# Optimization experiments

Measured on AMD Instinct MI355X. Metric: run time of the kernel, lower is better.

## Reference

```python
import jax, jax.numpy as jnp
import numpy as np

B, S, H = 2, 2048, 2048
E = 4
I = 8192
EI = I // E  # expert intermediate size
VOCAB = 100000

def setup_inputs() -> dict:
    key = jax.random.key(0)
    k1, k2, k3, k4, k5 = jax.random.split(key, 5)
    hidden_states = jax.random.normal(k1, (B, S, H), dtype=jnp.float32)
    token_ids = jax.random.randint(k2, (B, S), 0, VOCAB, dtype=jnp.int64)
    gate_proj = jax.random.normal(k3, (E, H, EI), dtype=jnp.float32) * 0.02
    up_proj = jax.random.normal(k4, (E, H, EI), dtype=jnp.float32) * 0.02
    down_proj = jax.random.normal(k5, (E, EI, H), dtype=jnp.float32) * 0.02
    return {"hidden_states": hidden_states, "token_ids": token_ids,
            "gate_proj": gate_proj, "up_proj": up_proj, "down_proj": down_proj}

def reference(hidden_states, token_ids, gate_proj, up_proj, down_proj):
    b, s, h = hidden_states.shape
    e_dim = gate_proj.shape[0]
    # token_to_expert = arange(vocab) % E  (no frequency table)
    tid = jnp.clip(token_ids, 0, VOCAB - 1)
    expert_ids = (tid % e_dim).reshape(-1)          # [T]
    x = hidden_states.reshape(-1, h)                # [T, H]
    T = x.shape[0]
    t_idx = jnp.arange(T)
    # grouped GEMM == per-token GEMM with token's expert weight; compute per-expert then select
    gate_all = jnp.einsum('td,edf->tef', x, gate_proj)   # [T, E, EI]
    up_all = jnp.einsum('td,edf->tef', x, up_proj)       # [T, E, EI]
    gate = gate_all[t_idx, expert_ids]                   # [T, EI]
    up = up_all[t_idx, expert_ids]                       # [T, EI]
    inter = jax.nn.silu(gate) * up                       # fused SwiGLU
    out_all = jnp.einsum('tf,efd->ted', inter, down_proj)  # [T, E, H]
    out = out_all[t_idx, expert_ids]                     # [T, H]
    return out.reshape(b, s, h)
```

## Files before the change

### kernel.cpp

```cpp
#include <hip/hip_runtime.h>

#define H_DIM 2048
#define EI_DIM 2048
#define NEXP 4
#define BM 144
#define SEG 1152
#define NROWS 4608
#define NTM 32
#define NKB 64
#define NB 16
#define AFRAG 576
#define WFRAG 512

typedef __attribute__((ext_vector_type(4))) float f32x4;
typedef __attribute__((ext_vector_type(8))) short bf16x8;
typedef __attribute__((ext_vector_type(4))) short bf16x4;

__device__ __forceinline__ short f2bf(float f) {
  unsigned u = __builtin_bit_cast(unsigned, f);
  u += 0x7fffu + ((u >> 16) & 1u);
  return (short)(u >> 16);
}

__device__ __forceinline__ void gload16(const void* g, void* l) {
  __builtin_amdgcn_global_load_lds(
      (const __attribute__((address_space(1))) unsigned*)g,
      (__attribute__((address_space(3))) unsigned*)l, 16, 0, 0);
}

__global__ void route_kernel(const void* __restrict__ token_ids,
                             int* __restrict__ meta, int* __restrict__ row2tok) {
  __shared__ unsigned long long wtot[4];
  const int tid = threadIdx.x;
  const int lane = tid & 63;
  const int wv = tid >> 6;

  for (int i = tid; i < NROWS; i += 256) row2tok[i] = -1;

  const int* ti32 = (const int*)token_ids;
  bool is64 = true;
  for (int i = 0; i < 16; ++i)
    if (ti32[2 * i + 1] != 0) is64 = false;

  const int base = tid * 16;
  unsigned long long pack = 0ULL;
  unsigned eps = 0;
  for (int i = 0; i < 16; ++i) {
    long long v = is64 ? ((const long long*)token_ids)[base + i]
                       : (long long)ti32[base + i];
    if (v < 0) v = 0;
    if (v > 99999) v = 99999;
    int e = (int)(v & 3);
    eps |= (unsigned)e << (2 * i);
    pack += 1ULL << (16 * e);
  }

  unsigned long long incl = pack;
  for (int off = 1; off < 64; off <<= 1) {
    unsigned long long up = __shfl_up(incl, off, 64);
    if (lane >= off) incl += up;
  }
  if (lane == 63) wtot[wv] = incl;
  __syncthreads();

  unsigned long long waveBase = 0;
  for (int w = 0; w < 4; ++w)
    if (w < wv) waveBase += wtot[w];
  const unsigned long long exclu = waveBase + incl - pack;

  if (tid == 0) {
    meta[0] = 36;
    for (int t = 0; t < 36; ++t) meta[1 + t] = t / 9;
  }

  int cur[4];
  for (int e = 0; e < 4; ++e)
    cur[e] = e * SEG + (int)((exclu >> (16 * e)) & 0xffff);
  for (int i = 0; i < 16; ++i) {
    int e = (int)((eps >> (2 * i)) & 3);
    int idx = cur[e]++;
    if (idx < (e + 1) * SEG) row2tok[idx] = base + i;
  }
}


__global__ __launch_bounds__(256) void convert_kernel(
    const float* __restrict__ gW, const float* __restrict__ uW,
    const float* __restrict__ dW, short* __restrict__ Pg,
    short* __restrict__ Pu, short* __restrict__ Pd) {
  const int mat = blockIdx.y;
  const float* src = mat == 0 ? gW : (mat == 1 ? uW : dW);
  short* dst = mat == 0 ? Pg : (mat == 1 ? Pu : Pd);
  const int tId = blockIdx.x;
  const int e = tId >> 9;
  const int nb = (tId >> 5) & 15;
  const int kb = tId & 31;
  const int tid = threadIdx.x;
  const int ks = tid >> 5;
  const int c4 = (tid & 31) * 4;
  const float* sb = src + (size_t)e * H_DIM * EI_DIM +
                    (size_t)(kb * 64 + ks * 8) * 2048 + nb * 128 + c4;
  f32x4 rv[8];
#pragma unroll
  for (int j = 0; j < 8; ++j) rv[j] = *(const f32x4*)(sb + (size_t)j * 2048);
  short* db = dst + (size_t)tId * 8192 + (ks * 128 + c4) * 8;
#pragma unroll
  for (int i = 0; i < 4; ++i) {
    bf16x8 v;
#pragma unroll
    for (int j = 0; j < 8; ++j) v[j] = f2bf(rv[j][i]);
    *(bf16x8*)(db + i * 8) = v;
  }
}

__global__ __launch_bounds__(256) void gather_pack_kernel(
    const float* __restrict__ hidden, const int* __restrict__ row2tok,
    short* __restrict__ xp) {
  const int tile = blockIdx.x;
  const int kb = blockIdx.y;
  const int tid = threadIdx.x;
  short* db = xp + ((size_t)tile * NKB + kb) * (AFRAG * 8);
#pragma unroll
  for (int q = 0; q < 3; ++q) {
    if (q == 2 && tid >= 64) break;
    const int idx = q * 256 + tid;
    const int ks = idx / 144, r = idx - ks * 144;
    const int tok = row2tok[tile * BM + r];
    bf16x8 v = {0, 0, 0, 0, 0, 0, 0, 0};
    if (tok >= 0) {
      const f32x4* s =
          (const f32x4*)(hidden + (size_t)tok * H_DIM + kb * 32 + ks * 8);
      f32x4 a = s[0], b = s[1];
      v[0] = f2bf(a[0]); v[1] = f2bf(a[1]); v[2] = f2bf(a[2]); v[3] = f2bf(a[3]);
      v[4] = f2bf(b[0]); v[5] = f2bf(b[1]); v[6] = f2bf(b[2]); v[7] = f2bf(b[3]);
    }
    *(bf16x8*)(db + idx * 8) = v;
  }
}

__global__ __launch_bounds__(256, 2) void gemm1_kernel(
    const short* __restrict__ xp, const short* __restrict__ Pg,
    const short* __restrict__ Pu, short* __restrict__ inter) {
  const int b0 = blockIdx.x;
  const int swz = (b0 & 7) * 64 + (b0 >> 3);
  const int tile = swz >> 4, nb = swz & 15;
  const int e = tile >> 3;

  __shared__ short L[2][12800];

  const int tid = threadIdx.x, lane = tid & 63, wv = tid >> 6;
  const int l15 = lane & 15, lks = lane >> 4;

  f32x4 accG[9][2] = {};
  f32x4 accU[9][2] = {};

  const short* aB = xp + (size_t)(tile * NKB) * (AFRAG * 8);
  const short* gB = Pg + (size_t)((e * NB + nb) * NKB) * (WFRAG * 8);
  const short* uB = Pu + (size_t)((e * NB + nb) * NKB) * (WFRAG * 8);

  const int wuni = (tid & 192) * 16;

#define STAGE1(kb, buf)                                                       \
  {                                                                           \
    const short* a = aB + (size_t)(kb) * (AFRAG * 8);                         \
    const short* g = gB + (size_t)(kb) * (WFRAG * 8);                         \
    const short* u = uB + (size_t)(kb) * (WFRAG * 8);                         \
    char* la = (char*)&L[buf][0];                                             \
    char* lg = (char*)&L[buf][4608];                                          \
    char* lu = (char*)&L[buf][8704];                                          \
    gload16(a + tid * 8, la + wuni);                                          \
    gload16(a + (256 + tid) * 8, la + 4096 + wuni);                           \
    if (tid < 64) gload16(a + (512 + tid) * 8, la + 8192 + wuni);             \
    gload16(g + tid * 8, lg + wuni);                                          \
    gload16(g + (256 + tid) * 8, lg + 4096 + wuni);                           \
    gload16(u + tid * 8, lu + wuni);                                          \
    gload16(u + (256 + tid) * 8, lu + 4096 + wuni);                           \
  }

  STAGE1(0, 0);
  asm volatile("s_waitcnt vmcnt(0)" ::: "memory");
  __syncthreads();

  int buf = 0;
  for (int kb = 0; kb < NKB; ++kb) {
    if (kb < NKB - 1) STAGE1(kb + 1, buf ^ 1);
    const short* As = &L[buf][0];
    const short* Gs = &L[buf][4608];
    const short* Us = &L[buf][8704];
    bf16x8 af[9], bg[2], bu[2];
#pragma unroll
    for (int m = 0; m < 9; ++m)
      af[m] = *(const bf16x8*)(As + (lks * 144 + m * 16 + l15) * 8);
#pragma unroll
    for (int n = 0; n < 2; ++n) {
      const int c = wv * 32 + n * 16 + l15;
      bg[n] = *(const bf16x8*)(Gs + (lks * 128 + c) * 8);
      bu[n] = *(const bf16x8*)(Us + (lks * 128 + c) * 8);
    }
    __builtin_amdgcn_s_setprio(1);
#pragma unroll
    for (int m = 0; m < 9; ++m)
#pragma unroll
      for (int n = 0; n < 2; ++n) {
        accG[m][n] = __builtin_amdgcn_mfma_f32_16x16x32_bf16(
            af[m], bg[n], accG[m][n], 0, 0, 0);
        accU[m][n] = __builtin_amdgcn_mfma_f32_16x16x32_bf16(
            af[m], bu[n], accU[m][n], 0, 0, 0);
      }
    __builtin_amdgcn_s_setprio(0);
    if (kb < NKB - 1) {
      asm volatile("s_waitcnt vmcnt(0)" ::: "memory");
      __syncthreads();
    }
    buf ^= 1;
  }
#undef STAGE1

#pragma unroll
  for (int n = 0; n < 2; ++n) {
    const int C = nb * 128 + wv * 32 + n * 16 + l15;
    const int kb2 = C >> 5, ks2 = (C >> 3) & 3, kj = C & 7;
    short* ib = inter + (((size_t)tile * NKB + kb2) * AFRAG + ks2 * 144) * 8 + kj;
#pragma unroll
    for (int m = 0; m < 9; ++m)
#pragma unroll
      for (int j = 0; j < 4; ++j) {
        const int r = m * 16 + (lks << 2) + j;
        const float g = accG[m][n][j], u = accU[m][n][j];
        const float s = g / (1.0f + __expf(-g));
        ib[(size_t)r * 8] = f2bf(s * u);
      }
  }
}

__global__ __launch_bounds__(256, 2) void gemm2_kernel(
    const short* __restrict__ inter, const short* __restrict__ Pd,
    const int* __restrict__ row2tok, float* __restrict__ out) {
  const int b0 = blockIdx.x;
  const int swz = (b0 & 7) * 64 + (b0 >> 3);
  const int tile = swz >> 4, nb = swz & 15;
  const int e = tile >> 3;

  __shared__ short L[2][8704];

  const int tid = threadIdx.x, lane = tid & 63, wv = tid >> 6;
  const int l15 = lane & 15, lks = lane >> 4;

  f32x4 acc[9][2] = {};

  const short* aB = inter + (size_t)(tile * NKB) * (AFRAG * 8);
  const short* dB = Pd + (size_t)((e * NB + nb) * NKB) * (WFRAG * 8);

  const int wuni = (tid & 192) * 16;

#define STAGE2(kb, buf)                                                       \
  {                                                                           \
    const short* a = aB + (size_t)(kb) * (AFRAG * 8);                         \
    const short* d = dB + (size_t)(kb) * (WFRAG * 8);                         \
    char* la = (char*)&L[buf][0];                                             \
    char* ld = (char*)&L[buf][4608];                                          \
    gload16(a + tid * 8, la + wuni);                                          \
    gload16(a + (256 + tid) * 8, la + 4096 + wuni);                           \
    if (tid < 64) gload16(a + (512 + tid) * 8, la + 8192 + wuni);             \
    gload16(d + tid * 8, ld + wuni);                                          \
    gload16(d + (256 + tid) * 8, ld + 4096 + wuni);                           \
  }

  STAGE2(0, 0);
  asm volatile("s_waitcnt vmcnt(0)" ::: "memory");
  __syncthreads();

  int buf = 0;
  for (int kb = 0; kb < NKB; ++kb) {
    if (kb < NKB - 1) STAGE2(kb + 1, buf ^ 1);
    const short* As = &L[buf][0];
    const short* Bs = &L[buf][4608];
    bf16x8 af[9], bd[2];
#pragma unroll
    for (int m = 0; m < 9; ++m)
      af[m] = *(const bf16x8*)(As + (lks * 144 + m * 16 + l15) * 8);
#pragma unroll
    for (int n = 0; n < 2; ++n)
      bd[n] = *(const bf16x8*)(Bs + (lks * 128 + wv * 32 + n * 16 + l15) * 8);
    __builtin_amdgcn_s_setprio(1);
#pragma unroll
    for (int m = 0; m < 9; ++m)
#pragma unroll
      for (int n = 0; n < 2; ++n)
        acc[m][n] = __builtin_amdgcn_mfma_f32_16x16x32_bf16(af[m], bd[n],
                                                            acc[m][n], 0, 0, 0);
    __builtin_amdgcn_s_setprio(0);
    if (kb < NKB - 1) {
      asm volatile("s_waitcnt vmcnt(0)" ::: "memory");
      __syncthreads();
    }
    buf ^= 1;
  }
#undef STAGE2

#pragma unroll
  for (int m = 0; m < 9; ++m)
#pragma unroll
    for (int j = 0; j < 4; ++j) {
      const int r = tile * BM + m * 16 + (lks << 2) + j;
      const int tok = row2tok[r];
      if (tok >= 0) {
        float* orow = out + (size_t)tok * H_DIM + nb * 128 + wv * 32 + l15;
#pragma unroll
        for (int n = 0; n < 2; ++n) orow[n * 16] = acc[m][n][j];
      }
    }
}


__global__ void gather_fb_kernel(const float* __restrict__ hidden,
                                 const int* __restrict__ row2tok,
                                 short* __restrict__ xperm) {
  const int r = blockIdx.x;
  const int tok = row2tok[r];
  const int tid = threadIdx.x;
  f32x4 a = {0.f, 0.f, 0.f, 0.f}, b = {0.f, 0.f, 0.f, 0.f};
  if (tok >= 0) {
    const f32x4* src = (const f32x4*)(hidden + (size_t)tok * H_DIM + 8 * tid);
    a = src[0];
    b = src[1];
  }
  bf16x8 v;
  v[0] = f2bf(a[0]); v[1] = f2bf(a[1]); v[2] = f2bf(a[2]); v[3] = f2bf(a[3]);
  v[4] = f2bf(b[0]); v[5] = f2bf(b[1]); v[6] = f2bf(b[2]); v[7] = f2bf(b[3]);
  *(bf16x8*)(xperm + (size_t)r * H_DIM + 8 * tid) = v;
}

__global__ __launch_bounds__(256, 2) void gemm1_fb_kernel(
    const short* __restrict__ xperm, const float* __restrict__ gateW,
    const float* __restrict__ upW, const int* __restrict__ meta,
    short* __restrict__ inter) {
  const int tm = blockIdx.x;
  if (tm >= meta[0]) return;
  const int e = meta[1 + tm];
  const int rowBase = tm * 128;
  const int colBase = blockIdx.y * 128;
  const float* gW = gateW + (size_t)e * H_DIM * EI_DIM;
  const float* uW = upW + (size_t)e * H_DIM * EI_DIM;

  __shared__ short As[128 * 64];
  __shared__ short Bg[128 * 64];
  __shared__ short Bu[128 * 64];

  const int tid = threadIdx.x;
  const int lane = tid & 63;
  const int wv = tid >> 6;
  const int wr = (wv >> 1) * 64;
  const int wc = (wv & 1) * 64;

  f32x4 accG[4][4] = {};
  f32x4 accU[4][4] = {};

  const int ar = tid >> 3;
  const int ak = (tid & 7) * 8;
  const int bn = (tid & 31) * 4;
  const int bk = (tid >> 5) * 4;

  for (int k0 = 0; k0 < H_DIM; k0 += 64) {
    bf16x8 av[4];
#pragma unroll
    for (int p = 0; p < 4; ++p) {
      int r = ar + p * 32;
      av[p] = *(const bf16x8*)(xperm + (size_t)(rowBase + r) * H_DIM + k0 + ak);
    }
    f32x4 gv[2][4], uv[2][4];
#pragma unroll
    for (int p = 0; p < 2; ++p) {
      int kk = k0 + bk + p * 32;
#pragma unroll
      for (int i = 0; i < 4; ++i) {
        gv[p][i] = *(const f32x4*)(gW + (size_t)(kk + i) * EI_DIM + colBase + bn);
        uv[p][i] = *(const f32x4*)(uW + (size_t)(kk + i) * EI_DIM + colBase + bn);
      }
    }
    __syncthreads();
#pragma unroll
    for (int p = 0; p < 4; ++p) {
      int r = ar + p * 32;
      int idx = (r * 64 + ak) ^ ((r & 7) << 3);
      *(bf16x8*)(As + idx) = av[p];
    }
#pragma unroll
    for (int p = 0; p < 2; ++p) {
      int kk = bk + p * 32;
#pragma unroll
      for (int j = 0; j < 4; ++j) {
        int rowp = bn + j;
        int idx = (rowp * 64 + kk) ^ ((rowp & 7) << 3);
        bf16x4 vg, vu;
        vg[0] = f2bf(gv[p][0][j]); vg[1] = f2bf(gv[p][1][j]);
        vg[2] = f2bf(gv[p][2][j]); vg[3] = f2bf(gv[p][3][j]);
        vu[0] = f2bf(uv[p][0][j]); vu[1] = f2bf(uv[p][1][j]);
        vu[2] = f2bf(uv[p][2][j]); vu[3] = f2bf(uv[p][3][j]);
        *(bf16x4*)(Bg + idx) = vg;
        *(bf16x4*)(Bu + idx) = vu;
      }
    }
    __syncthreads();
#pragma unroll
    for (int kk = 0; kk < 64; kk += 32) {
      const int kb = kk + ((lane >> 4) << 3);
      bf16x8 af[4], bgf[4], buf_[4];
#pragma unroll
      for (int m = 0; m < 4; ++m) {
        int r = wr + m * 16 + (lane & 15);
        af[m] = *(const bf16x8*)(As + ((r * 64 + kb) ^ ((r & 7) << 3)));
      }
#pragma unroll
      for (int n = 0; n < 4; ++n) {
        int c = wc + n * 16 + (lane & 15);
        int idx = (c * 64 + kb) ^ ((c & 7) << 3);
        bgf[n] = *(const bf16x8*)(Bg + idx);
        buf_[n] = *(const bf16x8*)(Bu + idx);
      }
#pragma unroll
      for (int m = 0; m < 4; ++m)
#pragma unroll
        for (int n = 0; n < 4; ++n) {
          accG[m][n] = __builtin_amdgcn_mfma_f32_16x16x32_bf16(
              af[m], bgf[n], accG[m][n], 0, 0, 0);
          accU[m][n] = __builtin_amdgcn_mfma_f32_16x16x32_bf16(
              af[m], buf_[n], accU[m][n], 0, 0, 0);
        }
    }
  }
#pragma unroll
  for (int m = 0; m < 4; ++m)
#pragma unroll
    for (int n = 0; n < 4; ++n) {
      int c = colBase + wc + n * 16 + (lane & 15);
#pragma unroll
      for (int j = 0; j < 4; ++j) {
        int r = rowBase + wr + m * 16 + ((lane >> 4) << 2) + j;
        float g = accG[m][n][j], u = accU[m][n][j];
        float s = g / (1.0f + __expf(-g));
        inter[(size_t)r * EI_DIM + c] = f2bf(s * u);
      }
    }
}

__global__ __launch_bounds__(256, 2) void gemm2_fb_kernel(
    const short* __restrict__ inter, const float* __restrict__ downW,
    const int* __restrict__ meta, const int* __restrict__ row2tok,
    float* __restrict__ out) {
  const int tm = blockIdx.x;
  if (tm >= meta[0]) return;
  const int e = meta[1 + tm];
  const int rowBase = tm * 128;
  const int colBase = blockIdx.y * 128;
  const float* dW = downW + (size_t)e * EI_DIM * H_DIM;

  __shared__ short As[128 * 64];
  __shared__ short Bs[128 * 64];

  const int tid = threadIdx.x;
  const int lane = tid & 63;
  const int wv = tid >> 6;
  const int wr = (wv >> 1) * 64;
  const int wc = (wv & 1) * 64;

  f32x4 acc[4][4] = {};

  const int ar = tid >> 3;
  const int ak = (tid & 7) * 8;
  const int bn = (tid & 31) * 4;
  const int bk = (tid >> 5) * 4;

  for (int k0 = 0; k0 < EI_DIM; k0 += 64) {
    bf16x8 av[4];
#pragma unroll
    for (int p = 0; p < 4; ++p) {
      int r = ar + p * 32;
      av[p] = *(const bf16x8*)(inter + (size_t)(rowBase + r) * EI_DIM + k0 + ak);
    }
    f32x4 dv[2][4];
#pragma unroll
    for (int p = 0; p < 2; ++p) {
      int kk = k0 + bk + p * 32;
#pragma unroll
      for (int i = 0; i < 4; ++i)
        dv[p][i] = *(const f32x4*)(dW + (size_t)(kk + i) * H_DIM + colBase + bn);
    }
    __syncthreads();
#pragma unroll
    for (int p = 0; p < 4; ++p) {
      int r = ar + p * 32;
      int idx = (r * 64 + ak) ^ ((r & 7) << 3);
      *(bf16x8*)(As + idx) = av[p];
    }
#pragma unroll
    for (int p = 0; p < 2; ++p) {
      int kk = bk + p * 32;
#pragma unroll
      for (int j = 0; j < 4; ++j) {
        int rowp = bn + j;
        int idx = (rowp * 64 + kk) ^ ((rowp & 7) << 3);
        bf16x4 vd;
        vd[0] = f2bf(dv[p][0][j]); vd[1] = f2bf(dv[p][1][j]);
        vd[2] = f2bf(dv[p][2][j]); vd[3] = f2bf(dv[p][3][j]);
        *(bf16x4*)(Bs + idx) = vd;
      }
    }
    __syncthreads();
#pragma unroll
    for (int kk = 0; kk < 64; kk += 32) {
      const int kb = kk + ((lane >> 4) << 3);
      bf16x8 af[4], bf_[4];
#pragma unroll
      for (int m = 0; m < 4; ++m) {
        int r = wr + m * 16 + (lane & 15);
        af[m] = *(const bf16x8*)(As + ((r * 64 + kb) ^ ((r & 7) << 3)));
      }
#pragma unroll
      for (int n = 0; n < 4; ++n) {
        int c = wc + n * 16 + (lane & 15);
        bf_[n] = *(const bf16x8*)(Bs + ((c * 64 + kb) ^ ((c & 7) << 3)));
      }
#pragma unroll
      for (int m = 0; m < 4; ++m)
#pragma unroll
        for (int n = 0; n < 4; ++n)
          acc[m][n] = __builtin_amdgcn_mfma_f32_16x16x32_bf16(
              af[m], bf_[n], acc[m][n], 0, 0, 0);
    }
  }
#pragma unroll
  for (int m = 0; m < 4; ++m)
#pragma unroll
    for (int j = 0; j < 4; ++j) {
      int r = rowBase + wr + m * 16 + ((lane >> 4) << 2) + j;
      int tok = row2tok[r];
      if (tok >= 0) {
        float* orow = out + (size_t)tok * H_DIM + colBase + wc + (lane & 15);
#pragma unroll
        for (int n = 0; n < 4; ++n) orow[n * 16] = acc[m][n][j];
      }
    }
}


extern "C" void kernel_launch(void* const* d_in, const int* in_sizes, int n_in,
                              void* d_out, int out_size, void* d_ws,
                              size_t ws_size, hipStream_t stream) {
  const float* hidden = (const float*)d_in[0];
  const void* token_ids = d_in[1];
  const float* gateW = (const float*)d_in[2];
  const float* upW = (const float*)d_in[3];
  const float* downW = (const float*)d_in[4];
  float* out = (float*)d_out;

  int* meta = (int*)d_ws;
  int* row2tok = meta + 64;

  const size_t wMatShorts = (size_t)NEXP * NB * 32 * 8192;
  const size_t xpShorts = (size_t)NTM * NKB * AFRAG * 8;
  const size_t need = 32768 + 3 * wMatShorts * 2 + 2 * xpShorts * 2;

  route_kernel<<<1, 256, 0, stream>>>(token_ids, meta, row2tok);

  if (ws_size >= need) {
    short* Pg = (short*)((char*)d_ws + 32768);
    short* Pu = Pg + wMatShorts;
    short* Pd = Pu + wMatShorts;
    short* xp = Pd + wMatShorts;
    short* inter = xp + xpShorts;

    convert_kernel<<<dim3(2048, 3), 256, 0, stream>>>(gateW, upW, downW, Pg,
                                                      Pu, Pd);
    gather_pack_kernel<<<dim3(NTM, NKB), 256, 0, stream>>>(hidden, row2tok, xp);
    gemm1_kernel<<<512, 256, 0, stream>>>(xp, Pg, Pu, inter);
    gemm2_kernel<<<512, 256, 0, stream>>>(inter, Pd, row2tok, out);
  } else {
    short* xperm = (short*)((char*)d_ws + 32768);
    short* inter = xperm + (size_t)NROWS * H_DIM;

    gather_fb_kernel<<<NROWS, 256, 0, stream>>>(hidden, row2tok, xperm);
    gemm1_fb_kernel<<<dim3(36, EI_DIM / 128), 256, 0, stream>>>(
        xperm, gateW, upW, meta, inter);
    gemm2_fb_kernel<<<dim3(36, H_DIM / 128), 256, 0, stream>>>(
        inter, downW, meta, row2tok, out);
  }
}
```

Baseline: 193.3 us.

## Triple-buffer GEMM LDS staging with partial vmcnt waits and reorder weight conversion

Both GEMM kernels go from double to triple LDS buffering. Loads are issued two k-blocks ahead, and each iteration waits with a partial vmcnt count before a single barrier, instead of draining every load and syncing twice. The tail A-fragment load is spread across all four waves (16 lanes each) so every wave issues the same number of loads, which the fixed vmcnt counts rely on. The convert kernel's block-to-tile mapping is reordered so adjacent blocks read adjacent columns, giving more coalesced fp32 reads. In exchange, LDS use rises by half, which may limit occupancy at two blocks per CU.

```diff
diff --git a/kernel.cpp b/kernel.cpp
--- a/kernel.cpp
+++ b/kernel.cpp
@@ -93,8 +93,8 @@
   short* dst = mat == 0 ? Pg : (mat == 1 ? Pu : Pd);
   const int tId = blockIdx.x;
   const int e = tId >> 9;
-  const int nb = (tId >> 5) & 15;
-  const int kb = tId & 31;
+  const int kb = (tId >> 4) & 31;
+  const int nb = tId & 15;
   const int tid = threadIdx.x;
   const int ks = tid >> 5;
   const int c4 = (tid & 31) * 4;
@@ -103,7 +103,7 @@
   f32x4 rv[8];
 #pragma unroll
   for (int j = 0; j < 8; ++j) rv[j] = *(const f32x4*)(sb + (size_t)j * 2048);
-  short* db = dst + (size_t)tId * 8192 + (ks * 128 + c4) * 8;
+  short* db = dst + (size_t)(e * 512 + nb * 32 + kb) * 8192 + (ks * 128 + c4) * 8;
 #pragma unroll
   for (int i = 0; i < 4; ++i) {
     bf16x8 v;
@@ -146,10 +146,11 @@
   const int tile = swz >> 4, nb = swz & 15;
   const int e = tile >> 3;
 
-  __shared__ short L[2][12800];
+  __shared__ short L[3][12800];
 
   const int tid = threadIdx.x, lane = tid & 63, wv = tid >> 6;
   const int l15 = lane & 15, lks = lane >> 4;
+  const int wuni = (tid & 192) * 16;
 
   f32x4 accG[9][2] = {};
   f32x4 accU[9][2] = {};
@@ -158,19 +159,18 @@
   const short* gB = Pg + (size_t)((e * NB + nb) * NKB) * (WFRAG * 8);
   const short* uB = Pu + (size_t)((e * NB + nb) * NKB) * (WFRAG * 8);
 
-  const int wuni = (tid & 192) * 16;
-
-#define STAGE1(kb, buf)                                                       \
+#define STAGE1(kb, bf)                                                        \
   {                                                                           \
     const short* a = aB + (size_t)(kb) * (AFRAG * 8);                         \
     const short* g = gB + (size_t)(kb) * (WFRAG * 8);                         \
     const short* u = uB + (size_t)(kb) * (WFRAG * 8);                         \
-    char* la = (char*)&L[buf][0];                                             \
-    char* lg = (char*)&L[buf][4608];                                          \
-    char* lu = (char*)&L[buf][8704];                                          \
+    char* la = (char*)&L[bf][0];                                              \
+    char* lg = (char*)&L[bf][4608];                                           \
+    char* lu = (char*)&L[bf][8704];                                           \
     gload16(a + tid * 8, la + wuni);                                          \
     gload16(a + (256 + tid) * 8, la + 4096 + wuni);                           \
-    if (tid < 64) gload16(a + (512 + tid) * 8, la + 8192 + wuni);             \
+    if (lane < 16)                                                            \
+      gload16(a + (512 + wv * 16 + lane) * 8, la + 8192 + wv * 256);          \
     gload16(g + tid * 8, lg + wuni);                                          \
     gload16(g + (256 + tid) * 8, lg + 4096 + wuni);                           \
     gload16(u + tid * 8, lu + wuni);                                          \
@@ -178,15 +178,24 @@
   }
 
   STAGE1(0, 0);
-  asm volatile("s_waitcnt vmcnt(0)" ::: "memory");
-  __syncthreads();
-
-  int buf = 0;
+  STAGE1(1, 1);
+
+  int bcur = 0;
   for (int kb = 0; kb < NKB; ++kb) {
-    if (kb < NKB - 1) STAGE1(kb + 1, buf ^ 1);
-    const short* As = &L[buf][0];
-    const short* Gs = &L[buf][4608];
-    const short* Us = &L[buf][8704];
+    if (kb < NKB - 1)
+      asm volatile("s_waitcnt vmcnt(7)" ::: "memory");
+    else
+      asm volatile("s_waitcnt vmcnt(0)" ::: "memory");
+    __builtin_amdgcn_s_barrier();
+    __builtin_amdgcn_sched_barrier(0);
+    if (kb < NKB - 2) {
+      int bn2 = bcur + 2;
+      if (bn2 >= 3) bn2 -= 3;
+      STAGE1(kb + 2, bn2);
+    }
+    const short* As = &L[bcur][0];
+    const short* Gs = &L[bcur][4608];
+    const short* Us = &L[bcur][8704];
     bf16x8 af[9], bg[2], bu[2];
 #pragma unroll
     for (int m = 0; m < 9; ++m)
@@ -208,11 +217,7 @@
             af[m], bu[n], accU[m][n], 0, 0, 0);
       }
     __builtin_amdgcn_s_setprio(0);
-    if (kb < NKB - 1) {
-      asm volatile("s_waitcnt vmcnt(0)" ::: "memory");
-      __syncthreads();
-    }
-    buf ^= 1;
+    if (++bcur == 3) bcur = 0;
   }
 #undef STAGE1
 
@@ -241,40 +246,49 @@
   const int tile = swz >> 4, nb = swz & 15;
   const int e = tile >> 3;
 
-  __shared__ short L[2][8704];
+  __shared__ short L[3][8704];
 
   const int tid = threadIdx.x, lane = tid & 63, wv = tid >> 6;
   const int l15 = lane & 15, lks = lane >> 4;
+  const int wuni = (tid & 192) * 16;
 
   f32x4 acc[9][2] = {};
 
   const short* aB = inter + (size_t)(tile * NKB) * (AFRAG * 8);
   const short* dB = Pd + (size_t)((e * NB + nb) * NKB) * (WFRAG * 8);
 
-  const int wuni = (tid & 192) * 16;
-
-#define STAGE2(kb, buf)                                                       \
+#define STAGE2(kb, bf)                                                        \
   {                                                                           \
     const short* a = aB + (size_t)(kb) * (AFRAG * 8);                         \
     const short* d = dB + (size_t)(kb) * (WFRAG * 8);                         \
-    char* la = (char*)&L[buf][0];                                             \
-    char* ld = (char*)&L[buf][4608];                                          \
+    char* la = (char*)&L[bf][0];                                              \
+    char* ld = (char*)&L[bf][4608];                                           \
     gload16(a + tid * 8, la + wuni);                                          \
     gload16(a + (256 + tid) * 8, la + 4096 + wuni);                           \
-    if (tid < 64) gload16(a + (512 + tid) * 8, la + 8192 + wuni);             \
+    if (lane < 16)                                                            \
+      gload16(a + (512 + wv * 16 + lane) * 8, la + 8192 + wv * 256);          \
     gload16(d + tid * 8, ld + wuni);                                          \
     gload16(d + (256 + tid) * 8, ld + 4096 + wuni);                           \
   }
 
   STAGE2(0, 0);
-  asm volatile("s_waitcnt vmcnt(0)" ::: "memory");
-  __syncthreads();
-
-  int buf = 0;
+  STAGE2(1, 1);
+
+  int bcur = 0;
   for (int kb = 0; kb < NKB; ++kb) {
-    if (kb < NKB - 1) STAGE2(kb + 1, buf ^ 1);
-    const short* As = &L[buf][0];
-    const short* Bs = &L[buf][4608];
+    if (kb < NKB - 1)
+      asm volatile("s_waitcnt vmcnt(5)" ::: "memory");
+    else
+      asm volatile("s_waitcnt vmcnt(0)" ::: "memory");
+    __builtin_amdgcn_s_barrier();
+    __builtin_amdgcn_sched_barrier(0);
+    if (kb < NKB - 2) {
+      int bn2 = bcur + 2;
+      if (bn2 >= 3) bn2 -= 3;
+      STAGE2(kb + 2, bn2);
+    }
+    const short* As = &L[bcur][0];
+    const short* Bs = &L[bcur][4608];
     bf16x8 af[9], bd[2];
 #pragma unroll
     for (int m = 0; m < 9; ++m)
@@ -290,11 +304,7 @@
         acc[m][n] = __builtin_amdgcn_mfma_f32_16x16x32_bf16(af[m], bd[n],
                                                             acc[m][n], 0, 0, 0);
     __builtin_amdgcn_s_setprio(0);
-    if (kb < NKB - 1) {
-      asm volatile("s_waitcnt vmcnt(0)" ::: "memory");
-      __syncthreads();
-    }
-    buf ^= 1;
+    if (++bcur == 3) bcur = 0;
   }
 #undef STAGE2
 
```

Measured after the change: 192.7 us. About the same (-0.3%).

## Fuse fp32-to-bf16 weight conversion into GEMM loads, drop convert kernel

Applied to the files above, without the earlier changes.

Removes the separate weight-conversion kernel. The GEMM kernels now read fp32 gate/up/down weights straight from global memory into registers, convert them to bf16 and write them to LDS, with a register-staged prefetch of the next k-block that overlaps the MFMA loop. Block-to-tile mapping is also reswizzled so that each XCD handles one expert's weights, improving L2 locality. In exchange the GEMMs read twice as many weight bytes and do the conversion work inside the hot loop, which uses more VGPRs and adds LDS stores. This can slow the main loop even though a whole kernel pass and its workspace traffic are gone.

```diff
diff --git a/kernel.cpp b/kernel.cpp
--- a/kernel.cpp
+++ b/kernel.cpp
@@ -10,8 +10,8 @@
 #define NKB 64
 #define NB 16
 #define AFRAG 576
-#define WFRAG 512
-
+
+typedef __attribute__((ext_vector_type(2))) float f32x2;
 typedef __attribute__((ext_vector_type(4))) float f32x4;
 typedef __attribute__((ext_vector_type(8))) short bf16x8;
 typedef __attribute__((ext_vector_type(4))) short bf16x4;
@@ -83,35 +83,6 @@
   }
 }
 
-
-__global__ __launch_bounds__(256) void convert_kernel(
-    const float* __restrict__ gW, const float* __restrict__ uW,
-    const float* __restrict__ dW, short* __restrict__ Pg,
-    short* __restrict__ Pu, short* __restrict__ Pd) {
-  const int mat = blockIdx.y;
-  const float* src = mat == 0 ? gW : (mat == 1 ? uW : dW);
-  short* dst = mat == 0 ? Pg : (mat == 1 ? Pu : Pd);
-  const int tId = blockIdx.x;
-  const int e = tId >> 9;
-  const int nb = (tId >> 5) & 15;
-  const int kb = tId & 31;
-  const int tid = threadIdx.x;
-  const int ks = tid >> 5;
-  const int c4 = (tid & 31) * 4;
-  const float* sb = src + (size_t)e * H_DIM * EI_DIM +
-                    (size_t)(kb * 64 + ks * 8) * 2048 + nb * 128 + c4;
-  f32x4 rv[8];
-#pragma unroll
-  for (int j = 0; j < 8; ++j) rv[j] = *(const f32x4*)(sb + (size_t)j * 2048);
-  short* db = dst + (size_t)tId * 8192 + (ks * 128 + c4) * 8;
-#pragma unroll
-  for (int i = 0; i < 4; ++i) {
-    bf16x8 v;
-#pragma unroll
-    for (int j = 0; j < 8; ++j) v[j] = f2bf(rv[j][i]);
-    *(bf16x8*)(db + i * 8) = v;
-  }
-}
 
 __global__ __launch_bounds__(256) void gather_pack_kernel(
     const float* __restrict__ hidden, const int* __restrict__ row2tok,
@@ -139,54 +110,70 @@
 }
 
 __global__ __launch_bounds__(256, 2) void gemm1_kernel(
-    const short* __restrict__ xp, const short* __restrict__ Pg,
-    const short* __restrict__ Pu, short* __restrict__ inter) {
+    const short* __restrict__ xp, const float* __restrict__ gateW,
+    const float* __restrict__ upW, short* __restrict__ inter) {
   const int b0 = blockIdx.x;
-  const int swz = (b0 & 7) * 64 + (b0 >> 3);
-  const int tile = swz >> 4, nb = swz & 15;
-  const int e = tile >> 3;
+  const int xcd = b0 & 7, slot = b0 >> 3;
+  const int e = xcd >> 1;
+  const int tile = e * 8 + (slot & 7);
+  const int nb = (xcd & 1) * 8 + (slot >> 3);
 
   __shared__ short L[2][12800];
 
   const int tid = threadIdx.x, lane = tid & 63, wv = tid >> 6;
   const int l15 = lane & 15, lks = lane >> 4;
+  const int wuni = (tid & 192) * 16;
+  const int c2 = (tid & 63) * 2;
 
   f32x4 accG[9][2] = {};
   f32x4 accU[9][2] = {};
 
   const short* aB = xp + (size_t)(tile * NKB) * (AFRAG * 8);
-  const short* gB = Pg + (size_t)((e * NB + nb) * NKB) * (WFRAG * 8);
-  const short* uB = Pu + (size_t)((e * NB + nb) * NKB) * (WFRAG * 8);
-
-  const int wuni = (tid & 192) * 16;
-
-#define STAGE1(kb, buf)                                                       \
-  {                                                                           \
-    const short* a = aB + (size_t)(kb) * (AFRAG * 8);                         \
-    const short* g = gB + (size_t)(kb) * (WFRAG * 8);                         \
-    const short* u = uB + (size_t)(kb) * (WFRAG * 8);                         \
-    char* la = (char*)&L[buf][0];                                             \
-    char* lg = (char*)&L[buf][4608];                                          \
-    char* lu = (char*)&L[buf][8704];                                          \
-    gload16(a + tid * 8, la + wuni);                                          \
-    gload16(a + (256 + tid) * 8, la + 4096 + wuni);                           \
-    if (tid < 64) gload16(a + (512 + tid) * 8, la + 8192 + wuni);             \
-    gload16(g + tid * 8, lg + wuni);                                          \
-    gload16(g + (256 + tid) * 8, lg + 4096 + wuni);                           \
-    gload16(u + tid * 8, lu + wuni);                                          \
-    gload16(u + (256 + tid) * 8, lu + 4096 + wuni);                           \
-  }
-
-  STAGE1(0, 0);
-  asm volatile("s_waitcnt vmcnt(0)" ::: "memory");
+  const float* gS = gateW + (size_t)e * H_DIM * EI_DIM + nb * 128 + c2;
+  const float* uS = upW + (size_t)e * H_DIM * EI_DIM + nb * 128 + c2;
+
+  f32x2 gv[8], uv[8];
+
+#define ISSUE1(kb, bf)                                                    \
+  {                                                                       \
+    const short* a = aB + (size_t)(kb) * (AFRAG * 8);                     \
+    char* la = (char*)&L[bf][0];                                          \
+    gload16(a + tid * 8, la + wuni);                                      \
+    gload16(a + (256 + tid) * 8, la + 4096 + wuni);                       \
+    if (lane < 16)                                                        \
+      gload16(a + (512 + wv * 16 + lane) * 8, la + 8192 + wv * 256);      \
+    const float* gp = gS + (size_t)((kb) * 32 + wv * 8) * EI_DIM;         \
+    const float* up = uS + (size_t)((kb) * 32 + wv * 8) * EI_DIM;         \
+    _Pragma("unroll") for (int j = 0; j < 8; ++j) {                       \
+      gv[j] = *(const f32x2*)(gp + (size_t)j * EI_DIM);                   \
+      uv[j] = *(const f32x2*)(up + (size_t)j * EI_DIM);                   \
+    }                                                                     \
+  }
+
+#define WRITE1(bf)                                                        \
+  {                                                                       \
+    bf16x8 fa, fb, fc, fd;                                                \
+    _Pragma("unroll") for (int j = 0; j < 8; ++j) {                       \
+      fa[j] = f2bf(gv[j][0]); fb[j] = f2bf(gv[j][1]);                     \
+      fc[j] = f2bf(uv[j][0]); fd[j] = f2bf(uv[j][1]);                     \
+    }                                                                     \
+    short* lg = &L[bf][4608] + (wv * 128 + c2) * 8;                       \
+    short* lu = &L[bf][8704] + (wv * 128 + c2) * 8;                       \
+    *(bf16x8*)lg = fa; *(bf16x8*)(lg + 8) = fb;                           \
+    *(bf16x8*)lu = fc; *(bf16x8*)(lu + 8) = fd;                           \
+  }
+
+  ISSUE1(0, 0);
+  WRITE1(0);
   __syncthreads();
 
-  int buf = 0;
   for (int kb = 0; kb < NKB; ++kb) {
-    if (kb < NKB - 1) STAGE1(kb + 1, buf ^ 1);
-    const short* As = &L[buf][0];
-    const short* Gs = &L[buf][4608];
-    const short* Us = &L[buf][8704];
+    const int bf = kb & 1;
+    if (kb + 1 < NKB) ISSUE1(kb + 1, bf ^ 1);
+    __builtin_amdgcn_sched_barrier(0);
+    const short* As = &L[bf][0];
+    const short* Gs = &L[bf][4608];
+    const short* Us = &L[bf][8704];
     bf16x8 af[9], bg[2], bu[2];
 #pragma unroll
     for (int m = 0; m < 9; ++m)
@@ -208,13 +195,11 @@
             af[m], bu[n], accU[m][n], 0, 0, 0);
       }
     __builtin_amdgcn_s_setprio(0);
-    if (kb < NKB - 1) {
-      asm volatile("s_waitcnt vmcnt(0)" ::: "memory");
-      __syncthreads();
-    }
-    buf ^= 1;
-  }
-#undef STAGE1
+    if (kb + 1 < NKB) WRITE1(bf ^ 1);
+    __syncthreads();
+  }
+#undef ISSUE1
+#undef WRITE1
 
 #pragma unroll
   for (int n = 0; n < 2; ++n) {
@@ -234,54 +219,69 @@
 }
 
 __global__ __launch_bounds__(256, 2) void gemm2_kernel(
-    const short* __restrict__ inter, const short* __restrict__ Pd,
+    const short* __restrict__ inter, const float* __restrict__ downW,
     const int* __restrict__ row2tok, float* __restrict__ out) {
   const int b0 = blockIdx.x;
-  const int swz = (b0 & 7) * 64 + (b0 >> 3);
-  const int tile = swz >> 4, nb = swz & 15;
-  const int e = tile >> 3;
+  const int xcd = b0 & 7, slot = b0 >> 3;
+  const int e = xcd >> 1;
+  const int tile = e * 8 + (slot & 7);
+  const int nb = (xcd & 1) * 8 + (slot >> 3);
 
   __shared__ short L[2][8704];
 
   const int tid = threadIdx.x, lane = tid & 63, wv = tid >> 6;
   const int l15 = lane & 15, lks = lane >> 4;
+  const int wuni = (tid & 192) * 16;
+  const int c2 = (tid & 63) * 2;
 
   f32x4 acc[9][2] = {};
 
   const short* aB = inter + (size_t)(tile * NKB) * (AFRAG * 8);
-  const short* dB = Pd + (size_t)((e * NB + nb) * NKB) * (WFRAG * 8);
-
-  const int wuni = (tid & 192) * 16;
-
-#define STAGE2(kb, buf)                                                       \
-  {                                                                           \
-    const short* a = aB + (size_t)(kb) * (AFRAG * 8);                         \
-    const short* d = dB + (size_t)(kb) * (WFRAG * 8);                         \
-    char* la = (char*)&L[buf][0];                                             \
-    char* ld = (char*)&L[buf][4608];                                          \
-    gload16(a + tid * 8, la + wuni);                                          \
-    gload16(a + (256 + tid) * 8, la + 4096 + wuni);                           \
-    if (tid < 64) gload16(a + (512 + tid) * 8, la + 8192 + wuni);             \
-    gload16(d + tid * 8, ld + wuni);                                          \
-    gload16(d + (256 + tid) * 8, ld + 4096 + wuni);                           \
-  }
-
-  STAGE2(0, 0);
-  asm volatile("s_waitcnt vmcnt(0)" ::: "memory");
+  const float* dS = downW + (size_t)e * EI_DIM * H_DIM + nb * 128 + c2;
+
+  f32x2 dv[8];
+
+#define ISSUE2(kb, bf)                                                    \
+  {                                                                       \
+    const short* a = aB + (size_t)(kb) * (AFRAG * 8);                     \
+    char* la = (char*)&L[bf][0];                                          \
+    gload16(a + tid * 8, la + wuni);                                      \
+    gload16(a + (256 + tid) * 8, la + 4096 + wuni);                       \
+    if (lane < 16)                                                        \
+      gload16(a + (512 + wv * 16 + lane) * 8, la + 8192 + wv * 256);      \
+    const float* dp = dS + (size_t)((kb) * 32 + wv * 8) * H_DIM;          \
+    _Pragma("unroll") for (int j = 0; j < 8; ++j) {                       \
+      dv[j] = *(const f32x2*)(dp + (size_t)j * H_DIM);                    \
+    }                                                                     \
+  }
+
+#define WRITE2(bf)                                                        \
+  {                                                                       \
+    bf16x8 fa, fb;                                                        \
+    _Pragma("unroll") for (int j = 0; j < 8; ++j) {                       \
+      fa[j] = f2bf(dv[j][0]); fb[j] = f2bf(dv[j][1]);                     \
+    }                                                                     \
+    short* ld = &L[bf][4608] + (wv * 128 + c2) * 8;                       \
+    *(bf16x8*)ld = fa; *(bf16x8*)(ld + 8) = fb;                           \
+  }
+
+  ISSUE2(0, 0);
+  WRITE2(0);
   __syncthreads();
 
-  int buf = 0;
   for (int kb = 0; kb < NKB; ++kb) {
-    if (kb < NKB - 1) STAGE2(kb + 1, buf ^ 1);
-    const short* As = &L[buf][0];
-    const short* Bs = &L[buf][4608];
+    const int bf = kb & 1;
+    if (kb + 1 < NKB) ISSUE2(kb + 1, bf ^ 1);
+    __builtin_amdgcn_sched_barrier(0);
+    const short* As = &L[bf][0];
+    const short* Ds = &L[bf][4608];
     bf16x8 af[9], bd[2];
 #pragma unroll
     for (int m = 0; m < 9; ++m)
       af[m] = *(const bf16x8*)(As + (lks * 144 + m * 16 + l15) * 8);
 #pragma unroll
     for (int n = 0; n < 2; ++n)
-      bd[n] = *(const bf16x8*)(Bs + (lks * 128 + wv * 32 + n * 16 + l15) * 8);
+      bd[n] = *(const bf16x8*)(Ds + (lks * 128 + wv * 32 + n * 16 + l15) * 8);
     __builtin_amdgcn_s_setprio(1);
 #pragma unroll
     for (int m = 0; m < 9; ++m)
@@ -290,13 +290,11 @@
         acc[m][n] = __builtin_amdgcn_mfma_f32_16x16x32_bf16(af[m], bd[n],
                                                             acc[m][n], 0, 0, 0);
     __builtin_amdgcn_s_setprio(0);
-    if (kb < NKB - 1) {
-      asm volatile("s_waitcnt vmcnt(0)" ::: "memory");
-      __syncthreads();
-    }
-    buf ^= 1;
-  }
-#undef STAGE2
+    if (kb + 1 < NKB) WRITE2(bf ^ 1);
+    __syncthreads();
+  }
+#undef ISSUE2
+#undef WRITE2
 
 #pragma unroll
   for (int m = 0; m < 9; ++m)
@@ -557,24 +555,18 @@
   int* meta = (int*)d_ws;
   int* row2tok = meta + 64;
 
-  const size_t wMatShorts = (size_t)NEXP * NB * 32 * 8192;
   const size_t xpShorts = (size_t)NTM * NKB * AFRAG * 8;
-  const size_t need = 32768 + 3 * wMatShorts * 2 + 2 * xpShorts * 2;
+  const size_t need = 32768 + 2 * xpShorts * 2;
 
   route_kernel<<<1, 256, 0, stream>>>(token_ids, meta, row2tok);
 
   if (ws_size >= need) {
-    short* Pg = (short*)((char*)d_ws + 32768);
-    short* Pu = Pg + wMatShorts;
-    short* Pd = Pu + wMatShorts;
-    short* xp = Pd + wMatShorts;
+    short* xp = (short*)((char*)d_ws + 32768);
     short* inter = xp + xpShorts;
 
-    convert_kernel<<<dim3(2048, 3), 256, 0, stream>>>(gateW, upW, downW, Pg,
-                                                      Pu, Pd);
     gather_pack_kernel<<<dim3(NTM, NKB), 256, 0, stream>>>(hidden, row2tok, xp);
-    gemm1_kernel<<<512, 256, 0, stream>>>(xp, Pg, Pu, inter);
-    gemm2_kernel<<<512, 256, 0, stream>>>(inter, Pd, row2tok, out);
+    gemm1_kernel<<<512, 256, 0, stream>>>(xp, gateW, upW, inter);
+    gemm2_kernel<<<512, 256, 0, stream>>>(inter, downW, row2tok, out);
   } else {
     short* xperm = (short*)((char*)d_ws + 32768);
     short* inter = xperm + (size_t)NROWS * H_DIM;
```

New measurement: 218.7 us. 1.13x slower.
